# Optimization experiments

Measured on AMD Instinct MI355X. Metric: run time of the kernel, lower is better.

The kernel has to match this reference:

```python
import jax, jax.numpy as jnp
import numpy as np
import math

D_MODEL = 768
D_STATE = 16
D_CONV = 4
EXPAND = 2
D_INNER = EXPAND * D_MODEL
DT_RANK = math.ceil(D_MODEL / 16)
B_SZ, SEQ = 2, 2048


def setup_inputs() -> dict:
    key = jax.random.key(0)
    ks = jax.random.split(key, 10)
    s = 0.02
    inp = {
        "input_states": jax.random.normal(ks[0], (B_SZ, SEQ, D_MODEL), jnp.float32),
        "in_proj_w": jax.random.normal(ks[1], (2 * D_INNER, D_MODEL), jnp.float32) * s,
        "conv_w": jax.random.normal(ks[2], (D_INNER, 1, D_CONV), jnp.float32) * s,
        "conv_b": jnp.zeros((D_INNER,), jnp.float32),
        "x_proj_w": jax.random.normal(ks[3], (DT_RANK + 2 * D_STATE, D_INNER), jnp.float32) * s,
        "dt_proj_w": jax.random.normal(ks[4], (D_INNER, DT_RANK), jnp.float32) * s,
        "dt_proj_b": jax.random.normal(ks[5], (D_INNER,), jnp.float32) * 0.1,
        # S4D-real style init: A_log = log(1..d_state) per channel
        "A_log": jnp.log(jnp.broadcast_to(jnp.arange(1, D_STATE + 1, dtype=jnp.float32), (D_INNER, D_STATE))),
        "D": jnp.ones((D_INNER,), jnp.float32),
        "out_proj_w": jax.random.normal(ks[6], (D_MODEL, D_INNER), jnp.float32) * s,
        "context_len": 2,
    }
    return inp


def _silu(x):
    return x * jax.nn.sigmoid(x)


def _chain_tree_scan(w, x):
    # first-order linear recurrence h_t = w_t * h_{t-1} + x_t along last axis
    # (w_0 is ignored by construction of the associative combine)
    def comb(l, r):
        al, bl = l
        ar, br = r
        return (ar * al, ar * bl + br)
    _, h = jax.lax.associative_scan(comb, (w, x), axis=-1)
    return h


def reference(input_states, in_proj_w, conv_w, conv_b, x_proj_w,
              dt_proj_w, dt_proj_b, A_log, D, out_proj_w, context_len):
    # context_len == 2 -> chain-tree branch (identity BFS order, parent[i]=i-1)
    b, L, dm = input_states.shape
    di, n = A_log.shape[0], A_log.shape[1]

    proj = jnp.einsum('bld,ed->ble', input_states, in_proj_w)  # [b,l,2*di]
    proj = jnp.transpose(proj, (0, 2, 1))                      # [b,2*di,l]
    hidden, gate = jnp.split(proj, 2, axis=1)                  # each [b,di,l]

    # causal depthwise conv1d (pad left d_conv-1, truncate to seq_len)
    hidden = jax.lax.conv_general_dilated(
        hidden, conv_w, window_strides=(1,), padding=[(D_CONV - 1, 0)],
        dimension_numbers=('NCH', 'OIH', 'NCH'), feature_group_count=di)
    hidden = _silu(hidden + conv_b[None, :, None])             # [b,di,l]

    ssm = jnp.einsum('bdl,ed->ble', hidden, x_proj_w)          # [b,l,dt_rank+2n]
    dt, Bm, Cm = jnp.split(ssm, [DT_RANK, DT_RANK + n], axis=-1)
    dt = jax.nn.softplus(jnp.einsum('blr,dr->bld', dt, dt_proj_w) + dt_proj_b)
    dt = jnp.transpose(dt, (0, 2, 1))                          # [b,di,l]

    A = -jnp.exp(A_log.astype(jnp.float32))                    # [di,n]
    dA = jnp.exp(A[None, :, None, :] * dt[:, :, :, None])      # [b,di,l,n]
    dBu = dt[:, :, :, None] * Bm[:, None, :, :] * hidden[:, :, :, None]  # [b,di,l,n]

    # rearrange 'b d l n -> b (d n) l'
    w = jnp.transpose(dA, (0, 1, 3, 2)).reshape(b, di * n, L)
    fin = jnp.transpose(dBu, (0, 1, 3, 2)).reshape(b, di * n, L)

    fin_f = jnp.flip(fin, axis=-1)
    w_f = jnp.roll(jnp.flip(w, axis=-1), 1, axis=-1)

    h = _chain_tree_scan(w_f, fin_f)
    # feature_out2 (edge_weight == w_f via identity gather) * 0.3 + feature_out1
    fout = 1.3 * h

    fout = jnp.flip(fout, axis=-1)                              # [b,(d n),l]
    fout = fout.reshape(b, di, n, L)
    fout = jnp.transpose(fout, (0, 3, 1, 2))                    # [b,l,d,n]

    scan_out = jnp.einsum('bldn,bln->bld', fout, Cm)            # [b,l,di]
    scan_out = jnp.transpose(scan_out, (0, 2, 1))               # [b,di,l]

    y = scan_out + hidden * D[None, :, None]
    y = y * _silu(gate)
    out = jnp.einsum('bdl,ed->ble', y, out_proj_w)              # [b,l,d_model]
    return out
```

## Files before the change

kernel.cpp:

```cpp
#include <hip/hip_runtime.h>
#include <hip/hip_bf16.h>

#define DI     1536
#define DM     768
#define E2     3072
#define NST    16
#define LSEQ   2048
#define NB     2
#define NLB    4096
#define SSMW   80
#define DTRANK 48
#define NC     32
#define CP     64
#define LOG2E  1.44269504f

typedef unsigned short u16;
typedef unsigned int   u32;
typedef __attribute__((ext_vector_type(8))) __bf16 bf16x8;
typedef __attribute__((ext_vector_type(4))) float  f32x4;

__device__ __forceinline__ float b2f(u16 u) {
  union { u32 i; float f; } v; v.i = ((u32)u) << 16; return v.f;
}
__device__ __forceinline__ u16 f2b(float f) {
  union { float f; u32 i; } v; v.f = f;
  u32 r = v.i + 0x7FFFu + ((v.i >> 16) & 1u);
  return (u16)(r >> 16);
}
__device__ __forceinline__ void gld16(const u16* g, u16* l) {
  __builtin_amdgcn_global_load_lds(
      (const __attribute__((address_space(1))) void*)g,
      (__attribute__((address_space(3))) void*)l, 16, 0, 0);
}
__device__ __forceinline__ float silu_f(float x) {
  return x / (1.f + __expf(-x));
}
__device__ __forceinline__ float fexp2(float x) {
  return __builtin_amdgcn_exp2f(x);
}

#define B2F_LO(w) __uint_as_float(((u32)(w)) << 16)
#define B2F_HI(w) __uint_as_float(((u32)(w)) & 0xFFFF0000u)

#define ROWSUM16(p)                                                                               \
  asm("v_add_f32 %0, %1, %2 row_ror:8 row_mask:0xf bank_mask:0xf" : "=v"(p) : "v"(p), "v"(p));    \
  asm("v_add_f32 %0, %1, %2 row_ror:4 row_mask:0xf bank_mask:0xf" : "=v"(p) : "v"(p), "v"(p));    \
  asm("v_add_f32 %0, %1, %2 row_ror:2 row_mask:0xf bank_mask:0xf" : "=v"(p) : "v"(p), "v"(p));    \
  asm("v_add_f32 %0, %1, %2 row_ror:1 row_mask:0xf bank_mask:0xf" : "=v"(p) : "v"(p), "v"(p));

__global__ __launch_bounds__(256) void castall(const float* __restrict__ x_in,
                                               const float* __restrict__ w_in,
                                               const float* __restrict__ w_out,
                                               const float* __restrict__ w_x,
                                               const float* __restrict__ w_dt,
                                               const float* __restrict__ b_dt,
                                               u16* __restrict__ in_b,
                                               u16* __restrict__ win_b,
                                               u16* __restrict__ wout_b,
                                               u16* __restrict__ wx_b,
                                               u16* __restrict__ wdtp_b) {
  int i = (blockIdx.x * 256 + threadIdx.x) * 4;
  const int n1 = NLB * DM, n2 = n1 + E2 * DM, n3 = n2 + DM * DI, n4 = n3 + SSMW * DI;
  const int n5 = n4 + DI * 64;
  if (i >= n5) return;
  if (i >= n4) {
    int off = i - n4;
    u16 o[4];
#pragma unroll
    for (int j = 0; j < 4; j++) {
      int row = (off + j) >> 6, col = (off + j) & 63;
      float v = (col < 48) ? w_dt[row * 48 + col] : (col == 48 ? b_dt[row] : 0.f);
      o[j] = f2b(v);
    }
    uint2 pk; pk.x = (u32)o[0] | ((u32)o[1] << 16); pk.y = (u32)o[2] | ((u32)o[3] << 16);
    *(uint2*)(wdtp_b + off) = pk;
    return;
  }
  const float* src; u16* dst; int off;
  if (i < n1)      { src = x_in;  dst = in_b;   off = i; }
  else if (i < n2) { src = w_in;  dst = win_b;  off = i - n1; }
  else if (i < n3) { src = w_out; dst = wout_b; off = i - n2; }
  else             { src = w_x;   dst = wx_b;   off = i - n3; }
  float4 v = *(const float4*)(src + off);
  u32 lo = (u32)f2b(v.x) | ((u32)f2b(v.y) << 16);
  u32 hi = (u32)f2b(v.z) | ((u32)f2b(v.w) << 16);
  uint2 pk; pk.x = lo; pk.y = hi;
  *(uint2*)(dst + off) = pk;
}

template<int CMODE>
__global__ __launch_bounds__(256) void gemm_bt(const u16* __restrict__ A,
                                               const u16* __restrict__ B,
                                               void* __restrict__ Cp,
                                               int M, int N, int K) {
  __shared__ __align__(16) u16 a_s[128 * 32];
  __shared__ __align__(16) u16 b_s[128 * 32];
  __shared__ __align__(16) u16 t_s[(CMODE == 2) ? 64 * 128 : 1];
  const int tid = threadIdx.x, lane = tid & 63, w = tid >> 6;
  const int m0 = blockIdx.x * 128, n0 = blockIdx.y * 128;
  const int wm = w >> 1, wn = w & 1;
  f32x4 acc[4][4];
#pragma unroll
  for (int i = 0; i < 4; i++)
#pragma unroll
    for (int j = 0; j < 4; j++) acc[i][j] = (f32x4){0.f, 0.f, 0.f, 0.f};

  const int rA = lane >> 2;
  const int c8 = (lane & 3) * 8;
  const int fr = lane & 15;
  const int fk = (lane >> 4) * 8;

  for (int k0 = 0; k0 < K; k0 += 32) {
#pragma unroll
    for (int j = 0; j < 2; j++) {
      int rr = (w * 2 + j) * 16;
      gld16(A + (size_t)(m0 + rr + rA) * K + k0 + c8, a_s + rr * 32);
      gld16(B + (size_t)(n0 + rr + rA) * K + k0 + c8, b_s + rr * 32);
    }
    __syncthreads();
    bf16x8 af[4], bf[4];
#pragma unroll
    for (int mi = 0; mi < 4; mi++)
      af[mi] = *(const bf16x8*)(a_s + (wm * 64 + mi * 16 + fr) * 32 + fk);
#pragma unroll
    for (int ni = 0; ni < 4; ni++)
      bf[ni] = *(const bf16x8*)(b_s + (wn * 64 + ni * 16 + fr) * 32 + fk);
#pragma unroll
    for (int mi = 0; mi < 4; mi++)
#pragma unroll
      for (int ni = 0; ni < 4; ni++)
        acc[mi][ni] = __builtin_amdgcn_mfma_f32_16x16x32_bf16(
            af[mi], bf[ni], acc[mi][ni], 0, 0, 0);
    __syncthreads();
  }

  const int rbase = (lane >> 4) * 4, cbase = lane & 15;
  if (CMODE == 2) {
    u16* dt = (u16*)Cp;
#pragma unroll
    for (int pass = 0; pass < 2; ++pass) {
      if (wn == pass) {
#pragma unroll
        for (int mi = 0; mi < 4; mi++)
#pragma unroll
          for (int ni = 0; ni < 4; ni++)
#pragma unroll
            for (int j = 0; j < 4; j++) {
              int ml = wm * 64 + mi * 16 + rbase + j;
              int nl = ni * 16 + cbase;
              float v = acc[mi][ni][j];
              float sp = (v > 20.f) ? v : log1pf(__expf(v));
              t_s[nl * 128 + ml] = f2b(sp);
            }
      }
      __syncthreads();
      for (int c = tid; c < 64 * 16; c += 256) {
        int nl = c >> 4, q = c & 15;
        int n = n0 + pass * 64 + nl;
        *(uint4*)(dt + (size_t)n * DI + m0 + q * 8) = *(const uint4*)(&t_s[nl * 128 + q * 8]);
      }
      __syncthreads();
    }
    return;
  }
#pragma unroll
  for (int mi = 0; mi < 4; mi++)
#pragma unroll
    for (int ni = 0; ni < 4; ni++)
#pragma unroll
      for (int j = 0; j < 4; j++) {
        int m = m0 + wm * 64 + mi * 16 + rbase + j;
        int n = n0 + wn * 64 + ni * 16 + cbase;
        float v = acc[mi][ni][j];
        if (CMODE == 0) {
          u16* C = (u16*)Cp;
          C[((size_t)(n >> 11) * E2 + m) * LSEQ + (n & 2047)] = f2b(v);
        } else {
          float* C = (float*)Cp;
          C[(size_t)m * N + n] = v;
        }
      }
}

__global__ __launch_bounds__(256) void gemm_xproj(const u16* __restrict__ A,
                                                  const u16* __restrict__ B,
                                                  float* __restrict__ C,
                                                  u16* __restrict__ dtin) {
  __shared__ __align__(16) u16 a_s[128 * 32];
  __shared__ __align__(16) u16 b_s[128 * 32];
  const int tid = threadIdx.x, lane = tid & 63, w = tid >> 6;
  const int n0 = blockIdx.x * 128;
  const int K = DI;
  f32x4 acc[5][2];
#pragma unroll
  for (int i = 0; i < 5; i++) { acc[i][0] = (f32x4){0,0,0,0}; acc[i][1] = (f32x4){0,0,0,0}; }

  const int rA = lane >> 2;
  const int c8 = (lane & 3) * 8;
  const int fr = lane & 15;
  const int fk = (lane >> 4) * 8;

  for (int k0 = 0; k0 < K; k0 += 32) {
#pragma unroll
    for (int j = 0; j < 2; j++) {
      int rr = (w * 2 + j) * 16;
      gld16(A + (size_t)(rr + rA) * K + k0 + c8, a_s + rr * 32);
      gld16(B + (size_t)(n0 + rr + rA) * K + k0 + c8, b_s + rr * 32);
    }
    __syncthreads();
    bf16x8 af[5], bf[2];
#pragma unroll
    for (int mi = 0; mi < 5; mi++)
      af[mi] = *(const bf16x8*)(a_s + (mi * 16 + fr) * 32 + fk);
#pragma unroll
    for (int ni = 0; ni < 2; ni++)
      bf[ni] = *(const bf16x8*)(b_s + (w * 32 + ni * 16 + fr) * 32 + fk);
#pragma unroll
    for (int mi = 0; mi < 5; mi++)
#pragma unroll
      for (int ni = 0; ni < 2; ni++)
        acc[mi][ni] = __builtin_amdgcn_mfma_f32_16x16x32_bf16(
            af[mi], bf[ni], acc[mi][ni], 0, 0, 0);
    __syncthreads();
  }

  const int rbase = (lane >> 4) * 4, cbase = lane & 15;
#pragma unroll
  for (int mi = 0; mi < 5; mi++)
#pragma unroll
    for (int ni = 0; ni < 2; ni++)
#pragma unroll
      for (int j = 0; j < 4; j++) {
        int m = mi * 16 + rbase + j;
        int n = n0 + w * 32 + ni * 16 + cbase;
        float v = acc[mi][ni][j];
        C[(size_t)n * SSMW + m] = v;
        if (m < 64) {
          u16 dv = (m < 48) ? f2b(v) : (m == 48 ? f2b(1.0f) : (u16)0);
          dtin[(size_t)n * 64 + m] = dv;
        }
      }
}

__global__ __launch_bounds__(256) void conv_silu(const u16* __restrict__ proj,
                                                 const float* __restrict__ cw,
                                                 const float* __restrict__ cb,
                                                 u16* __restrict__ hidden) {
  __shared__ __align__(16) u16 in_s[64][96];
  __shared__ __align__(16) u16 o_s[64][64];
  const int t = threadIdx.x;
  const int d0 = blockIdx.x * 64, l0 = blockIdx.y * 64, bb = blockIdx.z;

  for (int c = t; c < 64 * 12; c += 256) {
    int r = c / 12, q = c % 12;
    int gl = l0 - 32 + q * 8;
    uint4 v;
    if (gl >= 0) v = *(const uint4*)(proj + ((size_t)bb * E2 + d0 + r) * LSEQ + gl);
    else         v = (uint4){0u, 0u, 0u, 0u};
    *(uint4*)(&in_s[r][q * 8]) = v;
  }
  __syncthreads();

  const int dd = t >> 2, ls = t & 3;
  const int d = d0 + dd;
  const float w0 = cw[d * 4 + 0], w1 = cw[d * 4 + 1], w2 = cw[d * 4 + 2], w3 = cw[d * 4 + 3];
  const float bias = cb[d];
#pragma unroll
  for (int i = 0; i < 16; i++) {
    int li = ls * 16 + i;
    int base = 32 + li - 3;
    float h = w0 * b2f(in_s[dd][base + 0]) + w1 * b2f(in_s[dd][base + 1]) +
              w2 * b2f(in_s[dd][base + 2]) + w3 * b2f(in_s[dd][base + 3]) + bias;
    o_s[li][dd] = f2b(silu_f(h));
  }
  __syncthreads();

  for (int c = t; c < 512; c += 256) {
    int r = c >> 3, q = c & 7;
    *(uint4*)(hidden + ((size_t)bb * LSEQ + l0 + r) * DI + d0 + q * 8) =
        *(const uint4*)(&o_s[r][q * 8]);
  }
}

__global__ __launch_bounds__(256) void scan_sum(const u16* __restrict__ dt,
                                                const u16* __restrict__ hidden,
                                                const float* __restrict__ ssm,
                                                const float* __restrict__ A_log,
                                                float* __restrict__ gsum,
                                                float* __restrict__ sdt) {
  __shared__ __align__(16) u16 dt_t[16][80];
  __shared__ __align__(16) u16 hid_t[16][80];
  __shared__ __align__(16) float B_t[16][68];
  const int t = threadIdx.x;
  const int d0 = blockIdx.x * 16, c = blockIdx.y, bb = blockIdx.z;
  const int dl = t >> 4, n = t & 15;
  const int d = d0 + dl;
  const int l0 = c * CP;
  {
    int r = t >> 2, q = t & 3;
    size_t lbrow = (size_t)bb * LSEQ + l0 + r;
    uint2 dv = *(const uint2*)(dt + lbrow * DI + d0 + q * 4);
    uint2 hv = *(const uint2*)(hidden + lbrow * DI + d0 + q * 4);
    float4 bv = *(const float4*)(ssm + lbrow * SSMW + 48 + q * 4);
    dt_t[q * 4 + 0][r] = (u16)dv.x;  dt_t[q * 4 + 1][r] = (u16)(dv.x >> 16);
    dt_t[q * 4 + 2][r] = (u16)dv.y;  dt_t[q * 4 + 3][r] = (u16)(dv.y >> 16);
    hid_t[q * 4 + 0][r] = (u16)hv.x; hid_t[q * 4 + 1][r] = (u16)(hv.x >> 16);
    hid_t[q * 4 + 2][r] = (u16)hv.y; hid_t[q * 4 + 3][r] = (u16)(hv.y >> 16);
    B_t[q * 4 + 0][r] = bv.x; B_t[q * 4 + 1][r] = bv.y;
    B_t[q * 4 + 2][r] = bv.z; B_t[q * 4 + 3][r] = bv.w;
  }
  const float An2 = -__expf(A_log[d * 16 + n]) * LOG2E;
  float dt_prev = (c == NC - 1) ? 0.f
                : b2f(dt[((size_t)bb * LSEQ + l0 + CP) * DI + d]);
  __syncthreads();
  float g = 0.f, sumdt = 0.f;
#define STEPS(dtv_, hv_, Bv_) {            \
    float dtv = dtv_;                      \
    float dA = fexp2(An2 * dt_prev);       \
    g = dtv * (Bv_) * (hv_) + dA * g;      \
    sumdt += dt_prev;                      \
    dt_prev = dtv; }
#pragma unroll
  for (int s = 7; s >= 0; --s) {
    uint4 d8 = *(const uint4*)(&dt_t[dl][s * 8]);
    uint4 h8 = *(const uint4*)(&hid_t[dl][s * 8]);
    f32x4 b0 = *(const f32x4*)(&B_t[n][s * 8]);
    f32x4 b1 = *(const f32x4*)(&B_t[n][s * 8 + 4]);
    STEPS(B2F_HI(d8.w), B2F_HI(h8.w), b1[3]);
    STEPS(B2F_LO(d8.w), B2F_LO(h8.w), b1[2]);
    STEPS(B2F_HI(d8.z), B2F_HI(h8.z), b1[1]);
    STEPS(B2F_LO(d8.z), B2F_LO(h8.z), b1[0]);
    STEPS(B2F_HI(d8.y), B2F_HI(h8.y), b0[3]);
    STEPS(B2F_LO(d8.y), B2F_LO(h8.y), b0[2]);
    STEPS(B2F_HI(d8.x), B2F_HI(h8.x), b0[1]);
    STEPS(B2F_LO(d8.x), B2F_LO(h8.x), b0[0]);
  }
#undef STEPS
  size_t idx = (((size_t)bb * NC + c) * DI + d) * 16 + n;
  gsum[idx] = g;
  sdt[idx]  = sumdt;
}

__global__ __launch_bounds__(256) void scan_carry(const float* __restrict__ gsum,
                                                  const float* __restrict__ sdt,
                                                  const float* __restrict__ A_log,
                                                  float* __restrict__ carry) {
  const int t = blockIdx.x * 256 + threadIdx.x;
  const int bb = blockIdx.y;
  const int d = t >> 4, n = t & 15;
  const float An2 = -__expf(A_log[d * 16 + n]) * LOG2E;
  float cg = 0.f;
  carry[(((size_t)bb * NC + NC - 1) * DI + d) * 16 + n] = 0.f;
  for (int c = NC - 2; c >= 0; --c) {
    size_t up = (((size_t)bb * NC + (c + 1)) * DI + d) * 16 + n;
    cg = gsum[up] + fexp2(An2 * sdt[up]) * cg;
    carry[(((size_t)bb * NC + c) * DI + d) * 16 + n] = cg;
  }
}

__global__ __launch_bounds__(256) void scan_apply(const u16* __restrict__ proj,
                                                  const u16* __restrict__ hidden,
                                                  const u16* __restrict__ dt,
                                                  const float* __restrict__ ssm,
                                                  const float* __restrict__ A_log,
                                                  const float* __restrict__ Dp,
                                                  const float* __restrict__ carry,
                                                  u16* __restrict__ y) {
  __shared__ __align__(16) u16 dt_t[16][80];
  __shared__ __align__(16) u16 hid_t[16][80];
  __shared__ __align__(16) u16 gate_t[16][80];
  __shared__ __align__(16) float B_t[16][68];
  __shared__ __align__(16) float C_t[16][68];
  __shared__ __align__(16) u16 y_s[64][16];
  const int t = threadIdx.x;
  const int d0 = blockIdx.x * 16, c = blockIdx.y, bb = blockIdx.z;
  const int dl = t >> 4, n = t & 15;
  const int d = d0 + dl;
  const int l0 = c * CP;
  {
    int r = t >> 2, q = t & 3;
    size_t lbrow = (size_t)bb * LSEQ + l0 + r;
    uint2 dv = *(const uint2*)(dt + lbrow * DI + d0 + q * 4);
    uint2 hv = *(const uint2*)(hidden + lbrow * DI + d0 + q * 4);
    float4 bv = *(const float4*)(ssm + lbrow * SSMW + 48 + q * 4);
    float4 cv = *(const float4*)(ssm + lbrow * SSMW + 64 + q * 4);
    dt_t[q * 4 + 0][r] = (u16)dv.x;  dt_t[q * 4 + 1][r] = (u16)(dv.x >> 16);
    dt_t[q * 4 + 2][r] = (u16)dv.y;  dt_t[q * 4 + 3][r] = (u16)(dv.y >> 16);
    hid_t[q * 4 + 0][r] = (u16)hv.x; hid_t[q * 4 + 1][r] = (u16)(hv.x >> 16);
    hid_t[q * 4 + 2][r] = (u16)hv.y; hid_t[q * 4 + 3][r] = (u16)(hv.y >> 16);
    B_t[q * 4 + 0][r] = bv.x; B_t[q * 4 + 1][r] = bv.y;
    B_t[q * 4 + 2][r] = bv.z; B_t[q * 4 + 3][r] = bv.w;
    C_t[q * 4 + 0][r] = cv.x; C_t[q * 4 + 1][r] = cv.y;
    C_t[q * 4 + 2][r] = cv.z; C_t[q * 4 + 3][r] = cv.w;
  }
  {
    int r = t >> 4, q = t & 15;
    *(uint2*)(&gate_t[r][q * 4]) =
        *(const uint2*)(proj + ((size_t)bb * E2 + DI + d0 + r) * LSEQ + l0 + q * 4);
  }
  const float An2 = -__expf(A_log[d * 16 + n]) * LOG2E;
  const float Dd = Dp[d];
  float g = carry[(((size_t)bb * NC + c) * DI + d) * 16 + n];
  float dt_prev = (c == NC - 1) ? 0.f
                : b2f(dt[((size_t)bb * LSEQ + l0 + CP) * DI + d]);
  __syncthreads();
  float pcap[4] = {0.f, 0.f, 0.f, 0.f};
  float hcap[4] = {0.f, 0.f, 0.f, 0.f};
#define STEPA(IDX, dtv_, hv_, Bv_, Cv_) {                  \
    float dtv = dtv_; float hvv = hv_;                     \
    float dA = fexp2(An2 * dt_prev);                       \
    g = dtv * (Bv_) * hvv + dA * g;                        \
    float p = g * (Cv_);                                   \
    ROWSUM16(p);                                           \
    if (n == ((IDX) & 15)) {                               \
      pcap[(IDX) >> 4] = p; hcap[(IDX) >> 4] = hvv;        \
    }                                                      \
    dt_prev = dtv; }
#pragma unroll
  for (int s = 7; s >= 0; --s) {
    uint4 d8 = *(const uint4*)(&dt_t[dl][s * 8]);
    uint4 h8 = *(const uint4*)(&hid_t[dl][s * 8]);
    f32x4 b0 = *(const f32x4*)(&B_t[n][s * 8]);
    f32x4 b1 = *(const f32x4*)(&B_t[n][s * 8 + 4]);
    f32x4 c0 = *(const f32x4*)(&C_t[n][s * 8]);
    f32x4 c1 = *(const f32x4*)(&C_t[n][s * 8 + 4]);
    STEPA(s * 8 + 7, B2F_HI(d8.w), B2F_HI(h8.w), b1[3], c1[3]);
    STEPA(s * 8 + 6, B2F_LO(d8.w), B2F_LO(h8.w), b1[2], c1[2]);
    STEPA(s * 8 + 5, B2F_HI(d8.z), B2F_HI(h8.z), b1[1], c1[1]);
    STEPA(s * 8 + 4, B2F_LO(d8.z), B2F_LO(h8.z), b1[0], c1[0]);
    STEPA(s * 8 + 3, B2F_HI(d8.y), B2F_HI(h8.y), b0[3], c0[3]);
    STEPA(s * 8 + 2, B2F_LO(d8.y), B2F_LO(h8.y), b0[2], c0[2]);
    STEPA(s * 8 + 1, B2F_HI(d8.x), B2F_HI(h8.x), b0[1], c0[1]);
    STEPA(s * 8 + 0, B2F_LO(d8.x), B2F_LO(h8.x), b0[0], c0[0]);
  }
#undef STEPA
#pragma unroll
  for (int j2 = 0; j2 < 4; ++j2) {
    float gv = b2f(gate_t[dl][n + 16 * j2]);
    float yv = (1.3f * pcap[j2] + hcap[j2] * Dd) * silu_f(gv);
    y_s[n + 16 * j2][dl] = f2b(yv);
  }
  __syncthreads();
  {
    int r = t >> 2, q = t & 3;
    *(uint2*)(y + ((size_t)bb * LSEQ + l0 + r) * DI + d0 + q * 4) =
        *(const uint2*)(&y_s[r][q * 4]);
  }
}

extern "C" void kernel_launch(void* const* d_in, const int* in_sizes, int n_in,
                              void* d_out, int out_size, void* d_ws, size_t ws_size,
                              hipStream_t stream) {
  const float* x_in   = (const float*)d_in[0];
  const float* w_in   = (const float*)d_in[1];
  const float* conv_w = (const float*)d_in[2];
  const float* conv_b = (const float*)d_in[3];
  const float* w_x    = (const float*)d_in[4];
  const float* w_dt   = (const float*)d_in[5];
  const float* b_dt   = (const float*)d_in[6];
  const float* A_log  = (const float*)d_in[7];
  const float* Dp     = (const float*)d_in[8];
  const float* w_out  = (const float*)d_in[9];
  float* outp = (float*)d_out;

  size_t off = 0;
  auto carve = [&](size_t bytes) {
    void* p = (char*)d_ws + off;
    off += (bytes + 255) & ~(size_t)255;
    return p;
  };
  u16*   in_b   = (u16*)  carve((size_t)NLB * DM * 2);
  u16*   win_b  = (u16*)  carve((size_t)E2 * DM * 2);
  u16*   wout_b = (u16*)  carve((size_t)DM * DI * 2);
  u16*   wx_b   = (u16*)  carve((size_t)SSMW * DI * 2);
  u16*   wdtp_b = (u16*)  carve((size_t)DI * 64 * 2);
  u16*   proj_b = (u16*)  carve((size_t)NB * E2 * LSEQ * 2);
  u16*   hid_b  = (u16*)  carve((size_t)NLB * DI * 2);
  float* ssm_b  = (float*)carve((size_t)NLB * SSMW * 4);
  u16*   dtin_b = (u16*)  carve((size_t)NLB * 64 * 2);
  u16*   dt_b   = (u16*)  carve((size_t)NLB * DI * 2);
  u16*   y_b    = (u16*)  carve((size_t)NLB * DI * 2);
  float* gsum_b = (float*)carve((size_t)NB * NC * DI * 16 * 4);
  float* sdt_b  = (float*)carve((size_t)NB * NC * DI * 16 * 4);
  float* car_b  = (float*)carve((size_t)NB * NC * DI * 16 * 4);

  const int ncast = NLB * DM + E2 * DM + DM * DI + SSMW * DI + DI * 64;
  castall<<<(ncast + 1023) / 1024, 256, 0, stream>>>(
      x_in, w_in, w_out, w_x, w_dt, b_dt, in_b, win_b, wout_b, wx_b, wdtp_b);

  gemm_bt<0><<<dim3(E2 / 128, NLB / 128), 256, 0, stream>>>(
      win_b, in_b, proj_b, E2, NLB, DM);
  conv_silu<<<dim3(DI / 64, LSEQ / 64, NB), 256, 0, stream>>>(
      proj_b, conv_w, conv_b, hid_b);
  gemm_xproj<<<NLB / 128, 256, 0, stream>>>(wx_b, hid_b, ssm_b, dtin_b);

  gemm_bt<2><<<dim3(DI / 128, NLB / 128), 256, 0, stream>>>(
      wdtp_b, dtin_b, dt_b, DI, NLB, 64);

  scan_sum<<<dim3(DI / 16, NC, NB), 256, 0, stream>>>(
      dt_b, hid_b, ssm_b, A_log, gsum_b, sdt_b);
  scan_carry<<<dim3(DI * 16 / 256, NB), 256, 0, stream>>>(
      gsum_b, sdt_b, A_log, car_b);
  scan_apply<<<dim3(DI / 16, NC, NB), 256, 0, stream>>>(
      proj_b, hid_b, dt_b, ssm_b, A_log, Dp, car_b, y_b);

  gemm_bt<1><<<dim3(NLB / 128, DM / 128), 256, 0, stream>>>(
      y_b, wout_b, outp, NLB, DM, DI);
}
```

Measured before the change: 326.2 us.

## Fuse dt projection and softplus into scan kernels via per-tile MFMA

Removes the separate dt_proj GEMM launch and its full [L,DI] bf16 dt buffer. Each scan_sum and scan_apply block now recomputes its 16-channel by 65-step dt tile from dtin and the dt weights with two small MFMAs, applies softplus, and writes it straight to LDS. It also switches softplus to hardware exp2/log2 intrinsics. The cost is recomputing the dt tile in both scan kernels plus one extra row for dt_prev. The dtin buffer is padded by 64 rows so the lookahead read stays in bounds.

```diff
diff --git a/kernel.cpp b/kernel.cpp
--- a/kernel.cpp
+++ b/kernel.cpp
@@ -13,6 +13,7 @@
 #define NC     32
 #define CP     64
 #define LOG2E  1.44269504f
+#define RLOG2E 0.69314718f
 
 typedef unsigned short u16;
 typedef unsigned int   u32;
@@ -35,8 +36,10 @@
 __device__ __forceinline__ float silu_f(float x) {
   return x / (1.f + __expf(-x));
 }
-__device__ __forceinline__ float fexp2(float x) {
-  return __builtin_amdgcn_exp2f(x);
+__device__ __forceinline__ float fexp2(float x) { return __builtin_amdgcn_exp2f(x); }
+__device__ __forceinline__ float flog2(float x) { return __builtin_amdgcn_logf(x); }
+__device__ __forceinline__ float softplus_f(float x) {
+  return (x > 20.f) ? x : flog2(1.f + fexp2(x * LOG2E)) * RLOG2E;
 }
 
 #define B2F_LO(w) __uint_as_float(((u32)(w)) << 16)
@@ -95,7 +98,6 @@
                                                int M, int N, int K) {
   __shared__ __align__(16) u16 a_s[128 * 32];
   __shared__ __align__(16) u16 b_s[128 * 32];
-  __shared__ __align__(16) u16 t_s[(CMODE == 2) ? 64 * 128 : 1];
   const int tid = threadIdx.x, lane = tid & 63, w = tid >> 6;
   const int m0 = blockIdx.x * 128, n0 = blockIdx.y * 128;
   const int wm = w >> 1, wn = w & 1;
@@ -135,34 +137,6 @@
   }
 
   const int rbase = (lane >> 4) * 4, cbase = lane & 15;
-  if (CMODE == 2) {
-    u16* dt = (u16*)Cp;
-#pragma unroll
-    for (int pass = 0; pass < 2; ++pass) {
-      if (wn == pass) {
-#pragma unroll
-        for (int mi = 0; mi < 4; mi++)
-#pragma unroll
-          for (int ni = 0; ni < 4; ni++)
-#pragma unroll
-            for (int j = 0; j < 4; j++) {
-              int ml = wm * 64 + mi * 16 + rbase + j;
-              int nl = ni * 16 + cbase;
-              float v = acc[mi][ni][j];
-              float sp = (v > 20.f) ? v : log1pf(__expf(v));
-              t_s[nl * 128 + ml] = f2b(sp);
-            }
-      }
-      __syncthreads();
-      for (int c = tid; c < 64 * 16; c += 256) {
-        int nl = c >> 4, q = c & 15;
-        int n = n0 + pass * 64 + nl;
-        *(uint4*)(dt + (size_t)n * DI + m0 + q * 8) = *(const uint4*)(&t_s[nl * 128 + q * 8]);
-      }
-      __syncthreads();
-    }
-    return;
-  }
 #pragma unroll
   for (int mi = 0; mi < 4; mi++)
 #pragma unroll
@@ -282,7 +256,26 @@
   }
 }
 
-__global__ __launch_bounds__(256) void scan_sum(const u16* __restrict__ dt,
+
+#define DT_TILE_MFMA(dtin, wdtp)                                                          \
+  {                                                                                       \
+    const u16* ar = dtin + ((size_t)bb * LSEQ + l0) * 64;                                 \
+    bf16x8 wb0 = *(const bf16x8*)(wdtp + (size_t)(d0 + fr) * 64 + fk);                    \
+    bf16x8 wb1 = *(const bf16x8*)(wdtp + (size_t)(d0 + fr) * 64 + 32 + fk);               \
+    for (int mt = wv; mt < 5; mt += 4) {                                                  \
+      bf16x8 a0 = *(const bf16x8*)(ar + (size_t)(mt * 16 + fr) * 64 + fk);                \
+      bf16x8 a1 = *(const bf16x8*)(ar + (size_t)(mt * 16 + fr) * 64 + 32 + fk);           \
+      f32x4 da = (f32x4){0.f, 0.f, 0.f, 0.f};                                             \
+      da = __builtin_amdgcn_mfma_f32_16x16x32_bf16(a0, wb0, da, 0, 0, 0);                 \
+      da = __builtin_amdgcn_mfma_f32_16x16x32_bf16(a1, wb1, da, 0, 0, 0);                 \
+      _Pragma("unroll")                                                                   \
+      for (int j = 0; j < 4; j++)                                                         \
+        dt_t[cbase][mt * 16 + rbase + j] = f2b(softplus_f(da[j]));                        \
+    }                                                                                     \
+  }
+
+__global__ __launch_bounds__(256) void scan_sum(const u16* __restrict__ dtin,
+                                                const u16* __restrict__ wdtp,
                                                 const u16* __restrict__ hidden,
                                                 const float* __restrict__ ssm,
                                                 const float* __restrict__ A_log,
@@ -296,23 +289,23 @@
   const int dl = t >> 4, n = t & 15;
   const int d = d0 + dl;
   const int l0 = c * CP;
+  const int lane = t & 63, wv = t >> 6;
+  const int fr = lane & 15, fk = (lane >> 4) * 8;
+  const int rbase = (lane >> 4) * 4, cbase = lane & 15;
   {
     int r = t >> 2, q = t & 3;
     size_t lbrow = (size_t)bb * LSEQ + l0 + r;
-    uint2 dv = *(const uint2*)(dt + lbrow * DI + d0 + q * 4);
     uint2 hv = *(const uint2*)(hidden + lbrow * DI + d0 + q * 4);
     float4 bv = *(const float4*)(ssm + lbrow * SSMW + 48 + q * 4);
-    dt_t[q * 4 + 0][r] = (u16)dv.x;  dt_t[q * 4 + 1][r] = (u16)(dv.x >> 16);
-    dt_t[q * 4 + 2][r] = (u16)dv.y;  dt_t[q * 4 + 3][r] = (u16)(dv.y >> 16);
     hid_t[q * 4 + 0][r] = (u16)hv.x; hid_t[q * 4 + 1][r] = (u16)(hv.x >> 16);
     hid_t[q * 4 + 2][r] = (u16)hv.y; hid_t[q * 4 + 3][r] = (u16)(hv.y >> 16);
     B_t[q * 4 + 0][r] = bv.x; B_t[q * 4 + 1][r] = bv.y;
     B_t[q * 4 + 2][r] = bv.z; B_t[q * 4 + 3][r] = bv.w;
   }
+  DT_TILE_MFMA(dtin, wdtp)
   const float An2 = -__expf(A_log[d * 16 + n]) * LOG2E;
-  float dt_prev = (c == NC - 1) ? 0.f
-                : b2f(dt[((size_t)bb * LSEQ + l0 + CP) * DI + d]);
   __syncthreads();
+  float dt_prev = (c == NC - 1) ? 0.f : b2f(dt_t[dl][64]);
   float g = 0.f, sumdt = 0.f;
 #define STEPS(dtv_, hv_, Bv_) {            \
     float dtv = dtv_;                      \
@@ -360,7 +353,8 @@
 
 __global__ __launch_bounds__(256) void scan_apply(const u16* __restrict__ proj,
                                                   const u16* __restrict__ hidden,
-                                                  const u16* __restrict__ dt,
+                                                  const u16* __restrict__ dtin,
+                                                  const u16* __restrict__ wdtp,
                                                   const float* __restrict__ ssm,
                                                   const float* __restrict__ A_log,
                                                   const float* __restrict__ Dp,
@@ -377,15 +371,15 @@
   const int dl = t >> 4, n = t & 15;
   const int d = d0 + dl;
   const int l0 = c * CP;
+  const int lane = t & 63, wv = t >> 6;
+  const int fr = lane & 15, fk = (lane >> 4) * 8;
+  const int rbase = (lane >> 4) * 4, cbase = lane & 15;
   {
     int r = t >> 2, q = t & 3;
     size_t lbrow = (size_t)bb * LSEQ + l0 + r;
-    uint2 dv = *(const uint2*)(dt + lbrow * DI + d0 + q * 4);
     uint2 hv = *(const uint2*)(hidden + lbrow * DI + d0 + q * 4);
     float4 bv = *(const float4*)(ssm + lbrow * SSMW + 48 + q * 4);
     float4 cv = *(const float4*)(ssm + lbrow * SSMW + 64 + q * 4);
-    dt_t[q * 4 + 0][r] = (u16)dv.x;  dt_t[q * 4 + 1][r] = (u16)(dv.x >> 16);
-    dt_t[q * 4 + 2][r] = (u16)dv.y;  dt_t[q * 4 + 3][r] = (u16)(dv.y >> 16);
     hid_t[q * 4 + 0][r] = (u16)hv.x; hid_t[q * 4 + 1][r] = (u16)(hv.x >> 16);
     hid_t[q * 4 + 2][r] = (u16)hv.y; hid_t[q * 4 + 3][r] = (u16)(hv.y >> 16);
     B_t[q * 4 + 0][r] = bv.x; B_t[q * 4 + 1][r] = bv.y;
@@ -398,12 +392,12 @@
     *(uint2*)(&gate_t[r][q * 4]) =
         *(const uint2*)(proj + ((size_t)bb * E2 + DI + d0 + r) * LSEQ + l0 + q * 4);
   }
+  DT_TILE_MFMA(dtin, wdtp)
   const float An2 = -__expf(A_log[d * 16 + n]) * LOG2E;
   const float Dd = Dp[d];
   float g = carry[(((size_t)bb * NC + c) * DI + d) * 16 + n];
-  float dt_prev = (c == NC - 1) ? 0.f
-                : b2f(dt[((size_t)bb * LSEQ + l0 + CP) * DI + d]);
   __syncthreads();
+  float dt_prev = (c == NC - 1) ? 0.f : b2f(dt_t[dl][64]);
   float pcap[4] = {0.f, 0.f, 0.f, 0.f};
   float hcap[4] = {0.f, 0.f, 0.f, 0.f};
 #define STEPA(IDX, dtv_, hv_, Bv_, Cv_) {                  \
@@ -477,8 +471,7 @@
   u16*   proj_b = (u16*)  carve((size_t)NB * E2 * LSEQ * 2);
   u16*   hid_b  = (u16*)  carve((size_t)NLB * DI * 2);
   float* ssm_b  = (float*)carve((size_t)NLB * SSMW * 4);
-  u16*   dtin_b = (u16*)  carve((size_t)NLB * 64 * 2);
-  u16*   dt_b   = (u16*)  carve((size_t)NLB * DI * 2);
+  u16*   dtin_b = (u16*)  carve((size_t)(NLB + 64) * 64 * 2);
   u16*   y_b    = (u16*)  carve((size_t)NLB * DI * 2);
   float* gsum_b = (float*)carve((size_t)NB * NC * DI * 16 * 4);
   float* sdt_b  = (float*)carve((size_t)NB * NC * DI * 16 * 4);
@@ -494,15 +487,12 @@
       proj_b, conv_w, conv_b, hid_b);
   gemm_xproj<<<NLB / 128, 256, 0, stream>>>(wx_b, hid_b, ssm_b, dtin_b);
 
-  gemm_bt<2><<<dim3(DI / 128, NLB / 128), 256, 0, stream>>>(
-      wdtp_b, dtin_b, dt_b, DI, NLB, 64);
-
   scan_sum<<<dim3(DI / 16, NC, NB), 256, 0, stream>>>(
-      dt_b, hid_b, ssm_b, A_log, gsum_b, sdt_b);
+      dtin_b, wdtp_b, hid_b, ssm_b, A_log, gsum_b, sdt_b);
   scan_carry<<<dim3(DI * 16 / 256, NB), 256, 0, stream>>>(
       gsum_b, sdt_b, A_log, car_b);
   scan_apply<<<dim3(DI / 16, NC, NB), 256, 0, stream>>>(
-      proj_b, hid_b, dt_b, ssm_b, A_log, Dp, car_b, y_b);
+      proj_b, hid_b, dtin_b, wdtp_b, ssm_b, A_log, Dp, car_b, y_b);
 
   gemm_bt<1><<<dim3(NLB / 128, DM / 128), 256, 0, stream>>>(
       y_b, wout_b, outp, NLB, DM, DI);
```

Result: faster. 298.0 us (-8.6%).
